# Kernel tuning notes

Hardware: AMD Instinct MI355X
Metric: run time of the kernel (lower is better)

Reference implementation:

```python
import jax, jax.numpy as jnp
import numpy as np
import math

B, S, HID, H = 2, 4096, 512, 8
D_K = HID // H


def setup_inputs() -> dict:
    key = jax.random.key(0)
    ks = jax.random.split(key, 8)
    inp = {
        "query": jax.random.normal(ks[0], (B, S, HID), dtype=jnp.float32),
        "key": jax.random.normal(ks[1], (B, S, HID), dtype=jnp.float32),
        "value": jax.random.normal(ks[2], (B, S, HID), dtype=jnp.float32),
        "mask": jax.random.randint(ks[3], (B, S), 0, 2, dtype=jnp.int32),
        # conv1d kernel_size=1, bias=False -> plain [out,in] weights (xavier-normal-ish)
        "Wq": jax.random.normal(ks[4], (HID, HID), dtype=jnp.float32) * (1.0 / math.sqrt(HID)),
        "Wk": jax.random.normal(ks[5], (HID, HID), dtype=jnp.float32) * (1.0 / math.sqrt(HID)),
        "Wv": jax.random.normal(ks[6], (HID, HID), dtype=jnp.float32) * (1.0 / math.sqrt(HID)),
        "Wo": jax.random.normal(ks[7], (HID, HID), dtype=jnp.float32) * (1.0 / math.sqrt(HID)),
    }
    return inp


def reference(query, key, value, mask, Wq, Wk, Wv, Wo):
    b, s, _ = query.shape
    # conv1d(k=1, bias=False) projection == x @ W.T; split heads -> [b,h,s,d_k]
    def proj(x, W):
        return jnp.einsum('bsd,ed->bse', x, W).reshape(b, s, H, D_K).transpose(0, 2, 1, 3)
    q, k, v = proj(query, Wq), proj(key, Wk), proj(value, Wv)
    # NOTE: original scales by 1/log(d_k), not 1/sqrt(d_k)
    score = jnp.einsum('bhqd,bhkd->bhqk', q, k) / math.log(D_K)
    m = mask.reshape(b, 1, 1, s)  # broadcast over heads and query positions
    score = jnp.where(m == 0, jnp.float32(-1e30), score)
    attn = jax.nn.softmax(score, axis=-1)  # dropout is identity in eval
    x = jnp.einsum('bhqk,bhkd->bhqd', attn, v)
    x = x.transpose(0, 2, 1, 3).reshape(b, s, HID)
    return jnp.einsum('bsd,ed->bse', x, Wo)
```

## Files before the change

### kernel.cpp

```cpp
#include <hip/hip_runtime.h>
#include <hip/hip_bf16.h>
#include <cstdint>
#include <cstddef>


namespace {

constexpr int kB = 2, kS = 4096, kHid = 512, kH = 8, kDk = 64;
constexpr int kBH = kB * kH;
constexpr int kM = kB * kS;

typedef __attribute__((ext_vector_type(8))) short short8;
typedef __attribute__((ext_vector_type(4))) float floatx4;
typedef unsigned short u16;

__device__ __forceinline__ u16 bf16rne(float f) {
    uint32_t u = __float_as_uint(f);
    u += 0x7fffu + ((u >> 16) & 1u);
    return (u16)(u >> 16);
}
__device__ __forceinline__ uint32_t pk2(float lo, float hi) {
#if __has_builtin(__builtin_amdgcn_cvt_pk_bf16_f32)
    typedef __attribute__((ext_vector_type(2))) __bf16 bf2;
    bf2 h = __builtin_amdgcn_cvt_pk_bf16_f32(lo, hi);
    return __builtin_bit_cast(uint32_t, h);
#else
    return ((uint32_t)bf16rne(hi) << 16) | (uint32_t)bf16rne(lo);
#endif
}
__device__ __forceinline__ float fexp2(float x) {
#if __has_builtin(__builtin_amdgcn_exp2f)
    return __builtin_amdgcn_exp2f(x);
#else
    return exp2f(x);
#endif
}

__global__ __launch_bounds__(256) void cvt_qw(const float* __restrict__ q,
    const float* __restrict__ k, const float* __restrict__ v,
    const float* __restrict__ w0, const float* __restrict__ w1,
    const float* __restrict__ w2, const float* __restrict__ w3,
    u16* __restrict__ xall, u16* __restrict__ wall) {
    const int bx = blockIdx.x;
    if (bx < 12288) {
        int z = bx >> 12;
        size_t i = (size_t)(bx & 4095) * 256 + threadIdx.x;
        const float* src = z == 0 ? q : (z == 1 ? k : v);
        float4 f = ((const float4*)src)[i];
        ushort4 o;
        o.x = bf16rne(f.x); o.y = bf16rne(f.y);
        o.z = bf16rne(f.z); o.w = bf16rne(f.w);
        ((ushort4*)(xall + (size_t)z * kM * kHid))[i] = o;
    } else {
        int r = bx - 12288;
        int z = r >> 8;
        size_t i = (size_t)(r & 255) * 256 + threadIdx.x;
        const float* src = z == 0 ? w0 : (z == 1 ? w1 : (z == 2 ? w2 : w3));
        float sc = (z == 0)
            ? (float)(1.4426950408889634 / (6.0 * 0.6931471805599453))
            : 1.0f;
        float4 f = ((const float4*)src)[i];
        ushort4 o;
        o.x = bf16rne(f.x * sc); o.y = bf16rne(f.y * sc);
        o.z = bf16rne(f.z * sc); o.w = bf16rne(f.w * sc);
        ((ushort4*)(wall + (size_t)z * kHid * kHid))[i] = o;
    }
}

__global__ __launch_bounds__(256) void cvt_mask(const int* __restrict__ mask,
    float* __restrict__ fb) {
    int i = blockIdx.x * 256 + threadIdx.x;
    fb[i] = mask[i] ? 0.0f : -1e30f;
}

__global__ __launch_bounds__(256, 3) void proj(const u16* __restrict__ xall,
    const u16* __restrict__ wall, u16* __restrict__ qp, u16* __restrict__ kp,
    u16* __restrict__ vt) {
    __shared__ float smt[4][16][68];
    const int z = blockIdx.z;
    const u16* x = xall + (size_t)z * kM * kHid;
    const u16* w = wall + (size_t)z * kHid * kHid;
    const int wv = threadIdx.x >> 6, lane = threadIdx.x & 63;
    const int quad = lane >> 4, l16 = lane & 15;
    const int mb = blockIdx.y * 128 + (wv >> 1) * 64;
    const int nb = blockIdx.x * 128 + (wv & 1) * 64;
    floatx4 acc[4][4] = {};
    const u16* xr = x + (size_t)(mb + l16) * kHid + quad * 8;
    const u16* wr = w + (size_t)(nb + l16) * kHid + quad * 8;
    for (int k0 = 0; k0 < kHid; k0 += 32) {
        short8 a[4], bt[4];
#pragma unroll
        for (int i = 0; i < 4; i++)
            a[i] = *(const short8*)(xr + (size_t)i * 16 * kHid + k0);
#pragma unroll
        for (int t = 0; t < 4; t++)
            bt[t] = *(const short8*)(wr + (size_t)t * 16 * kHid + k0);
#pragma unroll
        for (int i = 0; i < 4; i++)
#pragma unroll
        for (int t = 0; t < 4; t++)
            acc[i][t] = __builtin_amdgcn_mfma_f32_16x16x32_bf16(a[i], bt[t], acc[i][t], 0, 0, 0);
    }
    if (z < 2) {
        u16* dst = (z == 0) ? qp : kp;
        const int row16 = lane >> 2, cseg = (lane & 3) * 16;
#pragma unroll
        for (int i = 0; i < 4; i++) {
#pragma unroll
            for (int t = 0; t < 4; t++)
#pragma unroll
            for (int r = 0; r < 4; r++)
                smt[wv][quad * 4 + r][t * 16 + l16] = acc[i][t][r];
            __builtin_amdgcn_wave_barrier();
            const float* rp = &smt[wv][row16][cseg];
            float4 f0 = *(const float4*)(rp);
            float4 f1 = *(const float4*)(rp + 4);
            float4 f2 = *(const float4*)(rp + 8);
            float4 f3 = *(const float4*)(rp + 12);
            uint4 o0, o1;
            o0.x = pk2(f0.x, f0.y); o0.y = pk2(f0.z, f0.w);
            o0.z = pk2(f1.x, f1.y); o0.w = pk2(f1.z, f1.w);
            o1.x = pk2(f2.x, f2.y); o1.y = pk2(f2.z, f2.w);
            o1.z = pk2(f3.x, f3.y); o1.w = pk2(f3.z, f3.w);
            u16* dp = dst + (size_t)(mb + i * 16 + row16) * kHid + nb + cseg;
            *(uint4*)dp = o0;
            *(uint4*)(dp + 8) = o1;
            __builtin_amdgcn_wave_barrier();
        }
    } else {
#pragma unroll
        for (int i = 0; i < 4; i++)
#pragma unroll
        for (int t = 0; t < 4; t++) {
            int m0 = mb + i * 16 + quad * 4;
            int n = nb + t * 16 + l16;
            int b = m0 >> 12, s = m0 & (kS - 1);
            int h = n >> 6,   d = n & (kDk - 1);
            ushort4 o;
            o.x = bf16rne(acc[i][t][0]); o.y = bf16rne(acc[i][t][1]);
            o.z = bf16rne(acc[i][t][2]); o.w = bf16rne(acc[i][t][3]);
            *(ushort4*)(vt + ((size_t)(b * kH + h) * kDk + d) * kS + s) = o;
        }
    }
}

__global__ __launch_bounds__(512, 4) void attn(const u16* __restrict__ qp,
    const u16* __restrict__ kp, const u16* __restrict__ vt,
    const float* __restrict__ fbias, u16* __restrict__ xo) {
    union SmT {
        struct { u16 K[2][64][64]; u16 V[2][64][64]; u16 P[8][16][72]; } s;
        float ep[8][16][68];
    };
    __shared__ __align__(16) SmT sm;
    const int tid = threadIdx.x;
    const int wv = tid >> 6, lane = tid & 63;
    const int quad = lane >> 4, l16 = lane & 15;
    const int bh = blockIdx.y, b = bh >> 3, h = bh & 7;
    const int q0 = blockIdx.x * 128 + wv * 16;
    const u16* Qb = qp + (size_t)b * kS * kHid + h * 64;
    const u16* Kb = kp + (size_t)b * kS * kHid + h * 64;
    const u16* Vb = vt + (size_t)bh * kDk * kS;
    const float* fm = fbias + b * kS;

    short8 qf[2];
    qf[0] = *(const short8*)(Qb + (size_t)(q0 + l16) * kHid + quad * 8);
    qf[1] = *(const short8*)(Qb + (size_t)(q0 + l16) * kHid + 32 + quad * 8);

    floatx4 O[4] = {};
    float rs = 0.0f;

    const int srow = tid >> 3;
    const int sc   = (tid & 7) * 8;
    const int pc   = ((tid & 7) ^ (srow & 7)) * 8;
    const int cA = (quad ^ (l16 & 7)) * 8;

    short8 rk, rv;
    rk = *(const short8*)(Kb + (size_t)srow * kHid + sc);
    rv = *(const short8*)(Vb + (size_t)srow * kS + sc);
    *(short8*)&sm.s.K[0][srow][pc] = rk;
    *(short8*)&sm.s.V[0][srow][pc] = rv;
    rk = *(const short8*)(Kb + (size_t)(64 + srow) * kHid + sc);
    rv = *(const short8*)(Vb + (size_t)srow * kS + 64 + sc);
    __syncthreads();

    for (int it = 0; it < 64; ++it) {
        const int p = it & 1;
        const int kt = it * 64;
        *(short8*)&sm.s.K[1 - p][srow][pc] = rk;
        *(short8*)&sm.s.V[1 - p][srow][pc] = rv;
        {
            const int kt2 = ((it + 2) & 63) * 64;
            rk = *(const short8*)(Kb + (size_t)(kt2 + srow) * kHid + sc);
            rv = *(const short8*)(Vb + (size_t)srow * kS + kt2 + sc);
        }
        short8 kf[4][2], vf[4][2];
#pragma unroll
        for (int t = 0; t < 4; t++) {
            kf[t][0] = *(const short8*)&sm.s.K[p][t * 16 + l16][cA];
            kf[t][1] = *(const short8*)&sm.s.K[p][t * 16 + l16][cA ^ 32];
            vf[t][0] = *(const short8*)&sm.s.V[p][t * 16 + l16][cA];
            vf[t][1] = *(const short8*)&sm.s.V[p][t * 16 + l16][cA ^ 32];
        }
        floatx4 st[4];
#pragma unroll
        for (int t = 0; t < 4; t++) {
            floatx4 z = *(const floatx4*)(fm + kt + t * 16 + quad * 4);
            z = __builtin_amdgcn_mfma_f32_16x16x32_bf16(kf[t][0], qf[0], z, 0, 0, 0);
            st[t] = __builtin_amdgcn_mfma_f32_16x16x32_bf16(kf[t][1], qf[1], z, 0, 0, 0);
        }
        {
            u16* prow = &sm.s.P[wv][l16][0];
            float sum = 0.0f;
#pragma unroll
            for (int t = 0; t < 4; t++) {
                float p0 = fexp2(st[t][0]);
                float p1 = fexp2(st[t][1]);
                float p2 = fexp2(st[t][2]);
                float p3 = fexp2(st[t][3]);
                sum += (p0 + p1) + (p2 + p3);
                uint2 w2; w2.x = pk2(p0, p1); w2.y = pk2(p2, p3);
                *(uint2*)(prow + t * 16 + quad * 4) = w2;
            }
            rs += sum;
        }
        __builtin_amdgcn_wave_barrier();
        {
            short8 ap0 = *(const short8*)&sm.s.P[wv][l16][quad * 8];
            short8 ap1 = *(const short8*)&sm.s.P[wv][l16][32 + quad * 8];
#pragma unroll
            for (int td = 0; td < 4; td++) {
                O[td] = __builtin_amdgcn_mfma_f32_16x16x32_bf16(vf[td][0], ap0, O[td], 0, 0, 0);
                O[td] = __builtin_amdgcn_mfma_f32_16x16x32_bf16(vf[td][1], ap1, O[td], 0, 0, 0);
            }
        }
        __syncthreads();
    }

    float inv;
    {
        float r = rs;
        r += __shfl_xor(r, 16);
        r += __shfl_xor(r, 32);
        inv = 1.0f / r;
    }
#pragma unroll
    for (int td = 0; td < 4; td++) {
        floatx4 o4 = O[td];
        o4[0] *= inv; o4[1] *= inv; o4[2] *= inv; o4[3] *= inv;
        *(floatx4*)&sm.ep[wv][l16][td * 16 + quad * 4] = o4;
    }
    __builtin_amdgcn_wave_barrier();
    {
        const int qloc = lane >> 2, seg = (lane & 3) * 16;
        const float* row = &sm.ep[wv][qloc][seg];
        u16* orow = xo + ((size_t)(b * kS + q0 + qloc)) * kHid + h * 64 + seg;
#pragma unroll
        for (int j = 0; j < 2; j++) {
            float4 f0 = *(const float4*)(row + j * 8);
            float4 f1 = *(const float4*)(row + j * 8 + 4);
            uint4 o;
            o.x = pk2(f0.x, f0.y); o.y = pk2(f0.z, f0.w);
            o.z = pk2(f1.x, f1.y); o.w = pk2(f1.z, f1.w);
            *(uint4*)(orow + j * 8) = o;
        }
    }
}

__global__ __launch_bounds__(256, 3) void oproj(const u16* __restrict__ x,
    const u16* __restrict__ w, float* __restrict__ out) {
    const int wv = threadIdx.x >> 6, lane = threadIdx.x & 63;
    const int quad = lane >> 4, l16 = lane & 15;
    const int mb = blockIdx.y * 128 + (wv >> 1) * 64;
    const int nb = blockIdx.x * 128 + (wv & 1) * 64;
    floatx4 acc[4][4] = {};
    const u16* xr = x + (size_t)(mb + l16) * kHid + quad * 8;
    const u16* wr = w + (size_t)(nb + l16) * kHid + quad * 8;
    for (int k0 = 0; k0 < kHid; k0 += 32) {
        short8 a[4], bt[4];
#pragma unroll
        for (int i = 0; i < 4; i++)
            a[i] = *(const short8*)(xr + (size_t)i * 16 * kHid + k0);
#pragma unroll
        for (int t = 0; t < 4; t++)
            bt[t] = *(const short8*)(wr + (size_t)t * 16 * kHid + k0);
#pragma unroll
        for (int i = 0; i < 4; i++)
#pragma unroll
        for (int t = 0; t < 4; t++)
            acc[i][t] = __builtin_amdgcn_mfma_f32_16x16x32_bf16(a[i], bt[t], acc[i][t], 0, 0, 0);
    }
#pragma unroll
    for (int i = 0; i < 4; i++)
#pragma unroll
    for (int t = 0; t < 4; t++)
#pragma unroll
    for (int r = 0; r < 4; r++) {
        int m = mb + i * 16 + quad * 4 + r;
        int n = nb + t * 16 + l16;
        out[(size_t)m * kHid + n] = acc[i][t][r];
    }
}

}

extern "C" void kernel_launch(void* const* d_in, const int* in_sizes, int n_in,
                              void* d_out, int out_size, void* d_ws, size_t ws_size,
                              hipStream_t stream) {
    const float* q  = (const float*)d_in[0];
    const float* k  = (const float*)d_in[1];
    const float* v  = (const float*)d_in[2];
    const int* mask = (const int*)d_in[3];
    const float* w0 = (const float*)d_in[4];
    const float* w1 = (const float*)d_in[5];
    const float* w2 = (const float*)d_in[6];
    const float* w3 = (const float*)d_in[7];
    float* out = (float*)d_out;

    u16* ws   = (u16*)d_ws;
    u16* xall = ws;
    u16* wall = xall + (size_t)3 * kM * kHid;
    u16* qp   = wall + (size_t)4 * kHid * kHid;
    u16* kp   = qp + (size_t)kBH * kS * kDk;
    u16* vt   = kp + (size_t)kBH * kS * kDk;
    u16* xo   = xall;
    float* fbias = (float*)(xall + (size_t)kM * kHid);

    dim3 blk(256);
    cvt_qw <<<dim3(13312), blk, 0, stream>>>(q, k, v, w0, w1, w2, w3, xall, wall);
    proj   <<<dim3(kHid / 128, kM / 128, 3), blk, 0, stream>>>(xall, wall, qp, kp, vt);
    cvt_mask<<<dim3(kB * kS / 256), blk, 0, stream>>>(mask, fbias);
    attn   <<<dim3(kS / 128, kBH), dim3(512), 0, stream>>>(qp, kp, vt, fbias, xo);
    oproj  <<<dim3(kHid / 128, kM / 128), blk, 0, stream>>>(
        xo, wall + (size_t)3 * kHid * kHid, out);
}
```

Measured before the change: 268.1 us.

## Split attention KV range across two blocks with 32x32 MFMA and async LDS loads

The attention kernel now splits the key range in two along grid z (interleaved 64-key tiles), writes unnormalized bf16 partial outputs and row sums to workspace, and a new combine kernel adds the partials and normalizes. Each wave handles 32 queries using 32x32x16 bf16 MFMA, keeps P in registers via permlane32 swaps instead of going through LDS, and stages K/V with global_load_lds direct-to-LDS loads. The split aims to raise occupancy and parallelism, and the register-resident P removes LDS traffic. The cost is an extra kernel launch, extra workspace traffic and bf16 rounding of the partial outputs before they are combined.

Measured after the change: 268.4 us. Within noise of the previous version (+0.1%).

```diff
diff --git a/kernel.cpp b/kernel.cpp
--- a/kernel.cpp
+++ b/kernel.cpp
@@ -12,6 +12,8 @@
 
 typedef __attribute__((ext_vector_type(8))) short short8;
 typedef __attribute__((ext_vector_type(4))) float floatx4;
+typedef __attribute__((ext_vector_type(16))) float floatx16;
+typedef __attribute__((ext_vector_type(4))) unsigned int uintx4;
 typedef unsigned short u16;
 
 __device__ __forceinline__ u16 bf16rne(float f) {
@@ -34,6 +36,23 @@
 #else
     return exp2f(x);
 #endif
+}
+__device__ __forceinline__ float bf2f(u16 v) {
+    return __uint_as_float((uint32_t)v << 16);
+}
+__device__ __forceinline__ void plswap(uint32_t& a, uint32_t& b) {
+#if __has_builtin(__builtin_amdgcn_permlane32_swap)
+    typedef __attribute__((ext_vector_type(2))) unsigned int uint2v;
+    uint2v r = __builtin_amdgcn_permlane32_swap(a, b, false, false);
+    a = r[0]; b = r[1];
+#else
+    asm volatile("v_permlane32_swap_b32 %0, %1" : "+v"(a), "+v"(b));
+#endif
+}
+__device__ __forceinline__ void gload16(const void* g, void* l) {
+    __builtin_amdgcn_global_load_lds(
+        (const __attribute__((address_space(1))) void*)g,
+        (__attribute__((address_space(3))) void*)l, 16, 0, 0);
 }
 
 __global__ __launch_bounds__(256) void cvt_qw(const float* __restrict__ q,
@@ -144,126 +163,150 @@
     }
 }
 
-__global__ __launch_bounds__(512, 4) void attn(const u16* __restrict__ qp,
+__global__ __launch_bounds__(256, 4) void attn(const u16* __restrict__ qp,
     const u16* __restrict__ kp, const u16* __restrict__ vt,
-    const float* __restrict__ fbias, u16* __restrict__ xo) {
+    const float* __restrict__ fbias, u16* __restrict__ ows,
+    float* __restrict__ rsws) {
     union SmT {
-        struct { u16 K[2][64][64]; u16 V[2][64][64]; u16 P[8][16][72]; } s;
-        float ep[8][16][68];
+        struct { u16 K[2][64][64]; u16 V[2][64][64]; } s;
+        float ep[4][32][33];
     };
     __shared__ __align__(16) SmT sm;
     const int tid = threadIdx.x;
-    const int wv = tid >> 6, lane = tid & 63;
-    const int quad = lane >> 4, l16 = lane & 15;
+    const int wv = tid >> 6, l = tid & 63;
+    const int hf = l >> 5, q32 = l & 31, l7 = l & 7;
     const int bh = blockIdx.y, b = bh >> 3, h = bh & 7;
-    const int q0 = blockIdx.x * 128 + wv * 16;
+    const int kz = blockIdx.z;
+    const int q0 = blockIdx.x * 128 + wv * 32;
     const u16* Qb = qp + (size_t)b * kS * kHid + h * 64;
     const u16* Kb = kp + (size_t)b * kS * kHid + h * 64;
     const u16* Vb = vt + (size_t)bh * kDk * kS;
     const float* fm = fbias + b * kS;
 
-    short8 qf[2];
-    qf[0] = *(const short8*)(Qb + (size_t)(q0 + l16) * kHid + quad * 8);
-    qf[1] = *(const short8*)(Qb + (size_t)(q0 + l16) * kHid + 32 + quad * 8);
-
-    floatx4 O[4] = {};
+    short8 qf[4];
+#pragma unroll
+    for (int m = 0; m < 4; m++)
+        qf[m] = *(const short8*)(Qb + (size_t)(q0 + q32) * kHid + m * 16 + hf * 8);
+
+    floatx16 O0 = {}, O1 = {};
     float rs = 0.0f;
 
-    const int srow = tid >> 3;
-    const int sc   = (tid & 7) * 8;
-    const int pc   = ((tid & 7) ^ (srow & 7)) * 8;
-    const int cA = (quad ^ (l16 & 7)) * 8;
-
-    short8 rk, rv;
-    rk = *(const short8*)(Kb + (size_t)srow * kHid + sc);
-    rv = *(const short8*)(Vb + (size_t)srow * kS + sc);
-    *(short8*)&sm.s.K[0][srow][pc] = rk;
-    *(short8*)&sm.s.V[0][srow][pc] = rv;
-    rk = *(const short8*)(Kb + (size_t)(64 + srow) * kHid + sc);
-    rv = *(const short8*)(Vb + (size_t)srow * kS + 64 + sc);
+    const int srow = l >> 3;
+    const int swcol = (l7 ^ srow) * 8;
+    auto stage = [&](int itn, int ph) {
+        const size_t kr = (size_t)(itn * 64 + wv * 8 + srow);
+        gload16(Kb + kr * kHid + swcol,        &sm.s.K[ph][wv * 8][0]);
+        gload16(Kb + (kr + 32) * kHid + swcol, &sm.s.K[ph][wv * 8 + 32][0]);
+        const size_t vr = (size_t)(wv * 8 + srow) * kS + itn * 64 + swcol;
+        gload16(Vb + vr,                       &sm.s.V[ph][wv * 8][0]);
+        gload16(Vb + (size_t)32 * kS + vr,     &sm.s.V[ph][wv * 8 + 32][0]);
+    };
+
+    stage(kz, 0);
     __syncthreads();
 
-    for (int it = 0; it < 64; ++it) {
-        const int p = it & 1;
-        const int kt = it * 64;
-        *(short8*)&sm.s.K[1 - p][srow][pc] = rk;
-        *(short8*)&sm.s.V[1 - p][srow][pc] = rv;
+    for (int s = 0; s < 32; ++s) {
+        const int it = kz + 2 * s, ph = s & 1, kt = it * 64;
+        if (s < 31) stage(it + 2, ph ^ 1);
+#pragma unroll
+        for (int ks = 0; ks < 2; ++ks) {
+            short8 kf[4];
+#pragma unroll
+            for (int m = 0; m < 4; m++)
+                kf[m] = *(const short8*)&sm.s.K[ph][ks * 32 + q32][((2 * m + hf) ^ l7) * 8];
+            short8 vf[2][2];
+#pragma unroll
+            for (int ds = 0; ds < 2; ds++)
+#pragma unroll
+            for (int tt = 0; tt < 2; tt++)
+                vf[ds][tt] = *(const short8*)&sm.s.V[ph][ds * 32 + q32][((ks * 4 + tt * 2 + hf) ^ l7) * 8];
+            floatx16 st;
+            {
+                const float* fp = fm + kt + ks * 32 + 4 * hf;
+                float4 g0 = *(const float4*)(fp);
+                float4 g1 = *(const float4*)(fp + 8);
+                float4 g2 = *(const float4*)(fp + 16);
+                float4 g3 = *(const float4*)(fp + 24);
+                st[0] = g0.x;  st[1] = g0.y;  st[2] = g0.z;  st[3] = g0.w;
+                st[4] = g1.x;  st[5] = g1.y;  st[6] = g1.z;  st[7] = g1.w;
+                st[8] = g2.x;  st[9] = g2.y;  st[10] = g2.z; st[11] = g2.w;
+                st[12] = g3.x; st[13] = g3.y; st[14] = g3.z; st[15] = g3.w;
+            }
+#pragma unroll
+            for (int m = 0; m < 4; m++)
+                st = __builtin_amdgcn_mfma_f32_32x32x16_bf16(kf[m], qf[m], st, 0, 0, 0);
+            float xx[16];
+#pragma unroll
+            for (int r = 0; r < 16; r++) xx[r] = fexp2(st[r]);
+            rs += (((xx[0] + xx[1]) + (xx[2] + xx[3])) + ((xx[4] + xx[5]) + (xx[6] + xx[7])))
+                + (((xx[8] + xx[9]) + (xx[10] + xx[11])) + ((xx[12] + xx[13]) + (xx[14] + xx[15])));
+            uint32_t w00 = pk2(xx[0], xx[1]),   w01 = pk2(xx[2], xx[3]);
+            uint32_t w10 = pk2(xx[4], xx[5]),   w11 = pk2(xx[6], xx[7]);
+            uint32_t w20 = pk2(xx[8], xx[9]),   w21 = pk2(xx[10], xx[11]);
+            uint32_t w30 = pk2(xx[12], xx[13]), w31 = pk2(xx[14], xx[15]);
+            plswap(w00, w10); plswap(w01, w11);
+            plswap(w20, w30); plswap(w21, w31);
+            uintx4 t0 = {w00, w01, w10, w11};
+            uintx4 t1 = {w20, w21, w30, w31};
+            short8 bf0 = __builtin_bit_cast(short8, t0);
+            short8 bf1 = __builtin_bit_cast(short8, t1);
+            O0 = __builtin_amdgcn_mfma_f32_32x32x16_bf16(vf[0][0], bf0, O0, 0, 0, 0);
+            O0 = __builtin_amdgcn_mfma_f32_32x32x16_bf16(vf[0][1], bf1, O0, 0, 0, 0);
+            O1 = __builtin_amdgcn_mfma_f32_32x32x16_bf16(vf[1][0], bf0, O1, 0, 0, 0);
+            O1 = __builtin_amdgcn_mfma_f32_32x32x16_bf16(vf[1][1], bf1, O1, 0, 0, 0);
+        }
+        __syncthreads();
+    }
+
+    rs += __shfl_xor(rs, 32);
+    if (hf == 0)
+        rsws[((size_t)kz * kBH + bh) * kS + q0 + q32] = rs;
+
+    u16* Ob = ows + (((size_t)kz * kBH + bh) * kS + q0) * kDk;
+#pragma unroll
+    for (int ds = 0; ds < 2; ds++) {
+#pragma unroll
+        for (int r = 0; r < 16; r++)
+            sm.ep[wv][q32][(r & 3) + 8 * (r >> 2) + 4 * hf] = (ds == 0) ? O0[r] : O1[r];
+        __builtin_amdgcn_wave_barrier();
         {
-            const int kt2 = ((it + 2) & 63) * 64;
-            rk = *(const short8*)(Kb + (size_t)(kt2 + srow) * kHid + sc);
-            rv = *(const short8*)(Vb + (size_t)srow * kS + kt2 + sc);
-        }
-        short8 kf[4][2], vf[4][2];
-#pragma unroll
-        for (int t = 0; t < 4; t++) {
-            kf[t][0] = *(const short8*)&sm.s.K[p][t * 16 + l16][cA];
-            kf[t][1] = *(const short8*)&sm.s.K[p][t * 16 + l16][cA ^ 32];
-            vf[t][0] = *(const short8*)&sm.s.V[p][t * 16 + l16][cA];
-            vf[t][1] = *(const short8*)&sm.s.V[p][t * 16 + l16][cA ^ 32];
-        }
-        floatx4 st[4];
-#pragma unroll
-        for (int t = 0; t < 4; t++) {
-            floatx4 z = *(const floatx4*)(fm + kt + t * 16 + quad * 4);
-            z = __builtin_amdgcn_mfma_f32_16x16x32_bf16(kf[t][0], qf[0], z, 0, 0, 0);
-            st[t] = __builtin_amdgcn_mfma_f32_16x16x32_bf16(kf[t][1], qf[1], z, 0, 0, 0);
-        }
-        {
-            u16* prow = &sm.s.P[wv][l16][0];
-            float sum = 0.0f;
-#pragma unroll
-            for (int t = 0; t < 4; t++) {
-                float p0 = fexp2(st[t][0]);
-                float p1 = fexp2(st[t][1]);
-                float p2 = fexp2(st[t][2]);
-                float p3 = fexp2(st[t][3]);
-                sum += (p0 + p1) + (p2 + p3);
-                uint2 w2; w2.x = pk2(p0, p1); w2.y = pk2(p2, p3);
-                *(uint2*)(prow + t * 16 + quad * 4) = w2;
-            }
-            rs += sum;
+            const int qq = l >> 1, c0 = (l & 1) * 16;
+            float f[16];
+#pragma unroll
+            for (int j = 0; j < 16; j++) f[j] = sm.ep[wv][qq][c0 + j];
+            uint4 o0, o1;
+            o0.x = pk2(f[0], f[1]);   o0.y = pk2(f[2], f[3]);
+            o0.z = pk2(f[4], f[5]);   o0.w = pk2(f[6], f[7]);
+            o1.x = pk2(f[8], f[9]);   o1.y = pk2(f[10], f[11]);
+            o1.z = pk2(f[12], f[13]); o1.w = pk2(f[14], f[15]);
+            u16* dp = Ob + (size_t)qq * kDk + ds * 32 + c0;
+            *(uint4*)dp = o0;
+            *(uint4*)(dp + 8) = o1;
         }
         __builtin_amdgcn_wave_barrier();
-        {
-            short8 ap0 = *(const short8*)&sm.s.P[wv][l16][quad * 8];
-            short8 ap1 = *(const short8*)&sm.s.P[wv][l16][32 + quad * 8];
-#pragma unroll
-            for (int td = 0; td < 4; td++) {
-                O[td] = __builtin_amdgcn_mfma_f32_16x16x32_bf16(vf[td][0], ap0, O[td], 0, 0, 0);
-                O[td] = __builtin_amdgcn_mfma_f32_16x16x32_bf16(vf[td][1], ap1, O[td], 0, 0, 0);
-            }
-        }
-        __syncthreads();
-    }
-
-    float inv;
-    {
-        float r = rs;
-        r += __shfl_xor(r, 16);
-        r += __shfl_xor(r, 32);
-        inv = 1.0f / r;
-    }
-#pragma unroll
-    for (int td = 0; td < 4; td++) {
-        floatx4 o4 = O[td];
-        o4[0] *= inv; o4[1] *= inv; o4[2] *= inv; o4[3] *= inv;
-        *(floatx4*)&sm.ep[wv][l16][td * 16 + quad * 4] = o4;
-    }
-    __builtin_amdgcn_wave_barrier();
-    {
-        const int qloc = lane >> 2, seg = (lane & 3) * 16;
-        const float* row = &sm.ep[wv][qloc][seg];
-        u16* orow = xo + ((size_t)(b * kS + q0 + qloc)) * kHid + h * 64 + seg;
-#pragma unroll
-        for (int j = 0; j < 2; j++) {
-            float4 f0 = *(const float4*)(row + j * 8);
-            float4 f1 = *(const float4*)(row + j * 8 + 4);
-            uint4 o;
-            o.x = pk2(f0.x, f0.y); o.y = pk2(f0.z, f0.w);
-            o.z = pk2(f1.x, f1.y); o.w = pk2(f1.z, f1.w);
-            *(uint4*)(orow + j * 8) = o;
-        }
-    }
+    }
+}
+
+__global__ __launch_bounds__(256) void combine(const u16* __restrict__ ows,
+    const float* __restrict__ rsws, u16* __restrict__ xo) {
+    size_t i = (size_t)blockIdx.x * 256 + threadIdx.x;
+    const int d8 = (int)(i & 7);
+    const int s  = (int)((i >> 3) & (kS - 1));
+    const int bh = (int)(i >> 15);
+    const int b = bh >> 3, h = bh & 7;
+    const size_t base = ((size_t)bh * kS + s) * kDk + d8 * 8;
+    short8 a = *(const short8*)(ows + base);
+    short8 c = *(const short8*)(ows + (size_t)kBH * kS * kDk + base);
+    float r = rsws[(size_t)bh * kS + s] + rsws[(size_t)kBH * kS + (size_t)bh * kS + s];
+    float inv = 1.0f / r;
+    float e[8];
+#pragma unroll
+    for (int j = 0; j < 8; j++)
+        e[j] = (bf2f((u16)a[j]) + bf2f((u16)c[j])) * inv;
+    uint4 o;
+    o.x = pk2(e[0], e[1]); o.y = pk2(e[2], e[3]);
+    o.z = pk2(e[4], e[5]); o.w = pk2(e[6], e[7]);
+    *(uint4*)(xo + ((size_t)b * kS + s) * kHid + h * 64 + d8 * 8) = o;
 }
 
 __global__ __launch_bounds__(256, 3) void oproj(const u16* __restrict__ x,
@@ -322,14 +365,17 @@
     u16* qp   = wall + (size_t)4 * kHid * kHid;
     u16* kp   = qp + (size_t)kBH * kS * kDk;
     u16* vt   = kp + (size_t)kBH * kS * kDk;
-    u16* xo   = xall;
-    float* fbias = (float*)(xall + (size_t)kM * kHid);
+    u16* ows  = xall;
+    float* fbias = (float*)(xall + (size_t)2 * kM * kHid);
+    float* rsws  = fbias + (size_t)kB * kS;
+    u16* xo   = qp;
 
     dim3 blk(256);
     cvt_qw <<<dim3(13312), blk, 0, stream>>>(q, k, v, w0, w1, w2, w3, xall, wall);
     proj   <<<dim3(kHid / 128, kM / 128, 3), blk, 0, stream>>>(xall, wall, qp, kp, vt);
     cvt_mask<<<dim3(kB * kS / 256), blk, 0, stream>>>(mask, fbias);
-    attn   <<<dim3(kS / 128, kBH), dim3(512), 0, stream>>>(qp, kp, vt, fbias, xo);
+    attn   <<<dim3(kS / 128, kBH, 2), blk, 0, stream>>>(qp, kp, vt, fbias, ows, rsws);
+    combine<<<dim3(2048), blk, 0, stream>>>(ows, rsws, xo);
     oproj  <<<dim3(kHid / 128, kM / 128), blk, 0, stream>>>(
         xo, wall + (size_t)3 * kHid * kHid, out);
 }
```
